# Kernel optimization log

Measured on AMD Instinct MI355X. Metric: run time of the kernel, lower is better.

The kernel has to match this reference:

```python
import jax, jax.numpy as jnp
import numpy as np

IN_CH = 31
OUT_CH = 31
G = 5          # grid_size
K = 3          # spline_order
GRID_LO, GRID_HI = -1.0, 1.0
NB = G + K     # number of B-spline basis functions
COEF_LEN = IN_CH * OUT_CH * NB        # 7688
UNIV_LEN = IN_CH * OUT_CH             # 961
RES_LEN = IN_CH * OUT_CH              # 961
PARAMS = COEF_LEN + UNIV_LEN + RES_LEN  # 9610


def _b_splines(x):
    """Cox-de Boor B-spline bases. x: (N, IN_CH) -> (N, IN_CH, G+K)."""
    h = (GRID_HI - GRID_LO) / G
    grid = jnp.arange(-K, G + K + 1, dtype=x.dtype) * h + GRID_LO  # (G+2K+1,)
    xe = x[..., None]
    b = ((xe >= grid[:-1]) & (xe < grid[1:])).astype(x.dtype)  # order-0, (N,I,G+2K)
    for p in range(1, K + 1):
        b = ((xe - grid[:-(p + 1)]) / (grid[p:-1] - grid[:-(p + 1)])) * b[..., :-1] \
          + ((grid[p + 1:] - xe) / (grid[p + 1:] - grid[1:-p])) * b[..., 1:]
    return b  # (N, IN_CH, NB)


def setup_inputs() -> dict:
    key = jax.random.key(0)
    k1, k2, k3 = jax.random.split(key, 3)
    # x in [-1,1) to span grid_range
    x = jax.random.uniform(k1, (1, IN_CH, 128, 128), dtype=jnp.float32) * 2.0 - 1.0
    # hypernetwork (generator) params: 3x3 conv 31 -> 9610
    gen_w = jax.random.normal(k2, (PARAMS, IN_CH, 3, 3), dtype=jnp.float32) * 0.02
    gen_b = jax.random.normal(k3, (PARAMS,), dtype=jnp.float32) * 0.01
    return {"x": x, "gen_w": gen_w, "gen_b": gen_b}


def reference(x, gen_w, gen_b):
    B, C, H, W = x.shape
    # generator: per-pixel KAN parameters, (B, PARAMS, H, W)
    w = jax.lax.conv_general_dilated(
        x, gen_w, window_strides=(1, 1), padding='SAME',
        dimension_numbers=('NCHW', 'OIHW', 'NCHW')) + gen_b[None, :, None, None]
    w = jnp.transpose(w, (0, 2, 3, 1)).reshape(B * H * W, PARAMS)
    xf = jnp.transpose(x, (0, 2, 3, 1)).reshape(B * H * W, C)
    # slice per-pixel params (mirrors kan_params_indices slicing + view)
    coef = w[:, :COEF_LEN].reshape(-1, IN_CH, OUT_CH, NB)
    univ = w[:, COEF_LEN:COEF_LEN + UNIV_LEN].reshape(-1, IN_CH, OUT_CH)
    res = w[:, COEF_LEN + UNIV_LEN:].reshape(-1, IN_CH, OUT_CH)
    bases = _b_splines(xf)                                # (N, I, NB)
    spline = jnp.einsum('nid,niod->nio', bases, coef)     # per-edge spline value
    silu = xf * jax.nn.sigmoid(xf)                        # residual activation
    out = jnp.einsum('nio,nio->no', univ, spline) + jnp.einsum('ni,nio->no', silu, res)
    return jnp.transpose(out.reshape(B, H, W, OUT_CH), (0, 3, 1, 2))
```

## Files before the change

### kernel.cpp

```cpp
#include <hip/hip_runtime.h>
#include <hip/hip_bf16.h>

#define OUT_CH   31
#define COEF_LEN 7688
#define NPIX     16384
#define CHUNKS   31
#define NFRG     24
#define NR       9
#define FRAG_U16 512
#define BP3_B    ((size_t)CHUNKS*NR*NFRG*FRAG_U16*2)
#define P1_B     ((size_t)OUT_CH*NPIX*4)
#define WS_NEED  (BP3_B + P1_B)

using f32x4 = __attribute__((ext_vector_type(4))) float;
using s16x8 = __attribute__((ext_vector_type(8))) short;

__device__ __forceinline__ unsigned short f2bf(float f) {
    unsigned int u = __float_as_uint(f);
    unsigned int r = (u + 0x7FFFu + ((u >> 16) & 1u)) >> 16;
    return (unsigned short)r;
}

__global__ void pack_kernel(const float* __restrict__ gw, const float* __restrict__ gb,
                            unsigned short* __restrict__ bp) {
    const int NMAIN = CHUNKS * NFRG * 64;
    int tt = blockIdx.x * 256 + threadIdx.x;
    if (tt >= NMAIN) return;
    int lane = tt & 63;
    int u = tt >> 6;
    int f = u % NFRG;
    int i = u / NFRG;
    int m = lane & 15, q8 = lane >> 4;
    int o = (m >> 2) * 8 + f / 3;
    int jslot = (f % 3) * 4 + (m & 3);
    int p = -1;
    if (o < OUT_CH && jslot < 10) {
        if (jslot < 8)       p = i * 248 + o * 8 + jslot;
        else if (jslot == 8) p = COEF_LEN + i * 31 + o;
        else                 p = COEF_LEN + 961 + i * 31 + o;
    }
    s16x8 vr[NR];
    #pragma unroll
    for (int r = 0; r < NR; ++r)
        #pragma unroll
        for (int jj = 0; jj < 8; ++jj) vr[r][jj] = 0;
    #pragma unroll
    for (int jj = 0; jj < 8; ++jj) {
        int ci = q8 * 8 + jj;
        if (p >= 0) {
            if (ci < 31) {
                const float* gr = gw + (long)p * 279 + ci * 9;
                #pragma unroll
                for (int r = 0; r < NR; ++r) vr[r][jj] = (short)f2bf(gr[r]);
            } else {
                vr[4][jj] = (short)f2bf(gb[p]);
            }
        }
    }
    #pragma unroll
    for (int r = 0; r < NR; ++r)
        *reinterpret_cast<s16x8*>(bp + (((size_t)i * NR + r) * NFRG + f) * FRAG_U16 + lane * 8) = vr[r];
}

__global__ void __launch_bounds__(512, 1)
main_kernel(const float* __restrict__ x, const unsigned short* __restrict__ bp3,
            float* __restrict__ dst0, float* __restrict__ dst1,
            int two_cg, int c0_in, int nc_in, int add_in) {
    __shared__ unsigned short slab[3 * 66 * 40];
    const int tid = threadIdx.x;
    const int bid = blockIdx.x;
    int row, ch, c0, nc, addf;
    float* dst;
    if (two_cg) {
        int cg = bid & 1;
        ch = (bid >> 1) & 1;
        row = bid >> 2;
        c0 = cg ? 16 : 0;
        nc = cg ? 15 : 16;
        dst = cg ? dst1 : dst0;
        addf = 0;
    } else {
        ch = bid & 1; row = bid >> 1;
        c0 = c0_in; nc = nc_in; dst = dst0; addf = add_in;
    }

    for (int idx = tid; idx < 3 * 66 * 40; idx += 512) {
        int slot = idx % 40;
        int t = idx / 40;
        int cc = t % 66;
        int rr = t / 66;
        int hh = row - 1 + rr, ww = ch * 64 - 1 + cc;
        unsigned short v = 0;
        if (slot < 31) {
            if ((unsigned)hh < 128u && (unsigned)ww < 128u)
                v = f2bf(x[slot * NPIX + hh * 128 + ww]);
        } else if (slot == 31) {
            v = 0x3F80;
        }
        slab[(rr * 66 + cc) * 40 + slot] = v;
    }
    __syncthreads();

    const int lane = tid & 63;
    const int fi = tid >> 6;
    const int q = lane >> 4;
    const int pix16 = lane & 15;
    const char* slabb = (const char*)slab;

    int sa[4];
    #pragma unroll
    for (int pg = 0; pg < 4; ++pg)
        sa[pg] = (pg * 16 + pix16) * 80 + q * 16;

    float oreg[4] = {0.f, 0.f, 0.f, 0.f};

    #pragma unroll 1
    for (int k = 0; k < nc; ++k) {
        const int ic = c0 + k;
        const unsigned short* aw = bp3 + ((size_t)ic * NR * NFRG + fi * 3) * FRAG_U16 + lane * 8;

        s16x8 pa[2][3];
        #pragma unroll
        for (int fl = 0; fl < 3; ++fl)
            pa[0][fl] = *reinterpret_cast<const s16x8*>(aw + fl * FRAG_U16);

        f32x4 acc[3][4];
        #pragma unroll
        for (int fl = 0; fl < 3; ++fl)
            #pragma unroll
            for (int pg = 0; pg < 4; ++pg)
                acc[fl][pg] = (f32x4){0.f, 0.f, 0.f, 0.f};

        #pragma unroll
        for (int r = 0; r < NR; ++r) {
            if (r + 1 < NR) {
                #pragma unroll
                for (int fl = 0; fl < 3; ++fl)
                    pa[(r + 1) & 1][fl] = *reinterpret_cast<const s16x8*>(
                        aw + ((r + 1) * NFRG + fl) * FRAG_U16);
            }
            const int roff = ((r / 3) * 66 + (r % 3)) * 80;
            s16x8 pbv[4];
            #pragma unroll
            for (int pg = 0; pg < 4; ++pg)
                pbv[pg] = *reinterpret_cast<const s16x8*>(slabb + sa[pg] + roff);

            __builtin_amdgcn_s_setprio(1);
            #pragma unroll
            for (int fl = 0; fl < 3; ++fl)
                #pragma unroll
                for (int pg = 0; pg < 4; ++pg)
                    acc[fl][pg] = __builtin_amdgcn_mfma_f32_16x16x32_bf16(
                        pa[r & 1][fl], pbv[pg], acc[fl][pg], 0, 0, 0);
            __builtin_amdgcn_s_setprio(0);
        }

        float bw0, bw1, bw2, bw3, cfv, slv;
        {
            unsigned short sv = slab[(66 + lane + 1) * 40 + ic];
            float xv = __uint_as_float((unsigned)sv << 16);
            float u5 = (xv + 1.0f) * 2.5f;
            cfv = fminf(fmaxf(floorf(u5), 0.f), 4.f);
            float t = u5 - cfv;
            float t2v = t * t, t3v = t2v * t;
            float omt = 1.f - t;
            bw3 = t3v * (1.f / 6.f);
            bw0 = omt * omt * omt * (1.f / 6.f);
            bw1 = 0.5f * t3v - t2v + (2.f / 3.f);
            bw2 = 1.f - bw0 - bw1 - bw3;
            slv = xv / (1.f + __expf(-xv));
        }

        #pragma unroll
        for (int pg = 0; pg < 4; ++pg) {
            const int src = pg * 16 + pix16;
            float b0 = __shfl(bw0, src);
            float b1 = __shfl(bw1, src);
            float b2 = __shfl(bw2, src);
            float b3 = __shfl(bw3, src);
            float cfp = __shfl(cfv, src);
            float slp = __shfl(slv, src);

            const float c0v = acc[0][pg][0], c1v = acc[0][pg][1];
            const float c2v = acc[0][pg][2], c3v = acc[0][pg][3];
            const float c4v = acc[1][pg][0], c5v = acc[1][pg][1];
            const float c6v = acc[1][pg][2], c7v = acc[1][pg][3];
            const bool m1 = cfp >= 1.f, m2 = cfp >= 2.f, m3 = cfp >= 3.f, m4 = cfp >= 4.f;
            float C0 = m1 ? c1v : c0v; C0 = m2 ? c2v : C0; C0 = m3 ? c3v : C0; C0 = m4 ? c4v : C0;
            float C1 = m1 ? c2v : c1v; C1 = m2 ? c3v : C1; C1 = m3 ? c4v : C1; C1 = m4 ? c5v : C1;
            float C2 = m1 ? c3v : c2v; C2 = m2 ? c4v : C2; C2 = m3 ? c5v : C2; C2 = m4 ? c6v : C2;
            float C3 = m1 ? c4v : c3v; C3 = m2 ? c5v : C3; C3 = m3 ? c6v : C3; C3 = m4 ? c7v : C3;

            float sp = b0 * C0;
            sp = fmaf(b1, C1, sp);
            sp = fmaf(b2, C2, sp);
            sp = fmaf(b3, C3, sp);
            oreg[pg] = fmaf(acc[2][pg][0], sp, fmaf(slp, acc[2][pg][1], oreg[pg]));
        }
    }

    const int o = q * 8 + fi;
    if (o < OUT_CH) {
        #pragma unroll
        for (int pg = 0; pg < 4; ++pg) {
            size_t gi = (size_t)o * NPIX + row * 128 + ch * 64 + pg * 16 + pix16;
            if (addf) dst[gi] += oreg[pg];
            else      dst[gi]  = oreg[pg];
        }
    }
}

__global__ void reduce_kernel(const float* __restrict__ p1, float* __restrict__ out) {
    int e = blockIdx.x * 256 + threadIdx.x;
    if (e < OUT_CH * NPIX) out[e] += p1[e];
}

extern "C" void kernel_launch(void* const* d_in, const int* in_sizes, int n_in,
                              void* d_out, int out_size, void* d_ws, size_t ws_size,
                              hipStream_t stream) {
    const float* x  = (const float*)d_in[0];
    const float* gw = (const float*)d_in[1];
    const float* gb = (const float*)d_in[2];
    float* outp = (float*)d_out;
    unsigned short* bpack = (unsigned short*)d_ws;
    float* p1 = (float*)((char*)d_ws + BP3_B);

    const int NMAIN = CHUNKS * NFRG * 64;
    pack_kernel<<<(NMAIN + 255) / 256, 256, 0, stream>>>(gw, gb, bpack);

    if (ws_size >= WS_NEED) {
        main_kernel<<<512, 512, 0, stream>>>(x, bpack, outp, p1, 1, 0, 0, 0);
        reduce_kernel<<<(OUT_CH * NPIX + 255) / 256, 256, 0, stream>>>(p1, outp);
    } else {
        main_kernel<<<256, 512, 0, stream>>>(x, bpack, outp, nullptr, 0, 0, 16, 0);
        main_kernel<<<256, 512, 0, stream>>>(x, bpack, outp, nullptr, 0, 16, 15, 1);
    }
}
```

Baseline: 114.5 us.

## Precompute spline weights in LDS and software-pipeline weight loads across channels

Before the main loop, the block now writes per-pixel, per-channel B-spline weights into LDS as a dense 8-wide weight row, along with the SiLU values. The epilogue then becomes a plain 8-term dot product instead of shuffles and select chains. The channel loop is unrolled by two, and the weight-fragment prefetch continues across channel boundaries so the next channel's first loads overlap the current epilogue. The cost is more LDS per block and extra global reads of x in the prologue.

```diff
diff --git a/kernel.cpp b/kernel.cpp
--- a/kernel.cpp
+++ b/kernel.cpp
@@ -8,7 +8,8 @@
 #define NFRG     24
 #define NR       9
 #define FRAG_U16 512
-#define BP3_B    ((size_t)CHUNKS*NR*NFRG*FRAG_U16*2)
+#define STEP_U16 (NFRG*FRAG_U16)
+#define BP3_B    ((size_t)CHUNKS*NR*STEP_U16*2)
 #define P1_B     ((size_t)OUT_CH*NPIX*4)
 #define WS_NEED  (BP3_B + P1_B)
 
@@ -67,6 +68,8 @@
             float* __restrict__ dst0, float* __restrict__ dst1,
             int two_cg, int c0_in, int nc_in, int add_in) {
     __shared__ unsigned short slab[3 * 66 * 40];
+    __shared__ float Wt[64 * 132];
+    __shared__ float SLt[64 * 17];
     const int tid = threadIdx.x;
     const int bid = blockIdx.x;
     int row, ch, c0, nc, addf;
@@ -99,7 +102,27 @@
         }
         slab[(rr * 66 + cc) * 40 + slot] = v;
     }
-    __syncthreads();
+
+    for (int idx = tid; idx < nc * 64; idx += 512) {
+        int px = idx & 63;
+        int k = idx >> 6;
+        float xv = x[(size_t)(c0 + k) * NPIX + row * 128 + ch * 64 + px];
+        float u5 = (xv + 1.0f) * 2.5f;
+        float cf = fminf(fmaxf(floorf(u5), 0.f), 4.f);
+        int ccb = (int)cf;
+        float t = u5 - cf;
+        float omt = 1.f - t;
+        float t2v = t * t, t3v = t2v * t;
+        float bw0 = omt * omt * omt * (1.f / 6.f);
+        float bw3 = t3v * (1.f / 6.f);
+        float bw1 = 0.5f * t3v - t2v + (2.f / 3.f);
+        float bw2 = 1.f - bw0 - bw1 - bw3;
+        float* wr = Wt + px * 132 + k * 8;
+        *reinterpret_cast<f32x4*>(wr) = (f32x4){0.f, 0.f, 0.f, 0.f};
+        *reinterpret_cast<f32x4*>(wr + 4) = (f32x4){0.f, 0.f, 0.f, 0.f};
+        wr[ccb] = bw0; wr[ccb + 1] = bw1; wr[ccb + 2] = bw2; wr[ccb + 3] = bw3;
+        SLt[px * 17 + k] = xv / (1.f + __expf(-xv));
+    }
 
     const int lane = tid & 63;
     const int fi = tid >> 6;
@@ -107,96 +130,93 @@
     const int pix16 = lane & 15;
     const char* slabb = (const char*)slab;
 
+    const unsigned short* awbase = bp3 + ((size_t)c0 * NR * NFRG + fi * 3) * FRAG_U16 + lane * 8;
+    s16x8 pa[2][3];
+    #pragma unroll
+    for (int fl = 0; fl < 3; ++fl)
+        pa[0][fl] = *reinterpret_cast<const s16x8*>(awbase + fl * FRAG_U16);
+
+    __syncthreads();
+
     int sa[4];
     #pragma unroll
     for (int pg = 0; pg < 4; ++pg)
         sa[pg] = (pg * 16 + pix16) * 80 + q * 16;
 
     float oreg[4] = {0.f, 0.f, 0.f, 0.f};
-
-    #pragma unroll 1
-    for (int k = 0; k < nc; ++k) {
-        const int ic = c0 + k;
-        const unsigned short* aw = bp3 + ((size_t)ic * NR * NFRG + fi * 3) * FRAG_U16 + lane * 8;
-
-        s16x8 pa[2][3];
+    f32x4 acc[3][4];
+
+    auto STEP = [&](int tl, int r, const unsigned short* awp, bool pf) {
+        if (pf) {
+            #pragma unroll
+            for (int fl = 0; fl < 3; ++fl)
+                pa[(tl + 1) & 1][fl] = *reinterpret_cast<const s16x8*>(
+                    awp + (size_t)(tl + 1) * STEP_U16 + fl * FRAG_U16);
+        }
+        const int roff = ((r / 3) * 66 + (r % 3)) * 80;
+        s16x8 pbv[4];
+        #pragma unroll
+        for (int pg = 0; pg < 4; ++pg)
+            pbv[pg] = *reinterpret_cast<const s16x8*>(slabb + sa[pg] + roff);
+        __builtin_amdgcn_s_setprio(1);
         #pragma unroll
         for (int fl = 0; fl < 3; ++fl)
-            pa[0][fl] = *reinterpret_cast<const s16x8*>(aw + fl * FRAG_U16);
-
-        f32x4 acc[3][4];
+            #pragma unroll
+            for (int pg = 0; pg < 4; ++pg)
+                acc[fl][pg] = __builtin_amdgcn_mfma_f32_16x16x32_bf16(
+                    pa[tl & 1][fl], pbv[pg], acc[fl][pg], 0, 0, 0);
+        __builtin_amdgcn_s_setprio(0);
+    };
+
+    auto ZERO = [&]() {
         #pragma unroll
         for (int fl = 0; fl < 3; ++fl)
             #pragma unroll
             for (int pg = 0; pg < 4; ++pg)
                 acc[fl][pg] = (f32x4){0.f, 0.f, 0.f, 0.f};
-
-        #pragma unroll
-        for (int r = 0; r < NR; ++r) {
-            if (r + 1 < NR) {
-                #pragma unroll
-                for (int fl = 0; fl < 3; ++fl)
-                    pa[(r + 1) & 1][fl] = *reinterpret_cast<const s16x8*>(
-                        aw + ((r + 1) * NFRG + fl) * FRAG_U16);
-            }
-            const int roff = ((r / 3) * 66 + (r % 3)) * 80;
-            s16x8 pbv[4];
-            #pragma unroll
-            for (int pg = 0; pg < 4; ++pg)
-                pbv[pg] = *reinterpret_cast<const s16x8*>(slabb + sa[pg] + roff);
-
-            __builtin_amdgcn_s_setprio(1);
-            #pragma unroll
-            for (int fl = 0; fl < 3; ++fl)
-                #pragma unroll
-                for (int pg = 0; pg < 4; ++pg)
-                    acc[fl][pg] = __builtin_amdgcn_mfma_f32_16x16x32_bf16(
-                        pa[r & 1][fl], pbv[pg], acc[fl][pg], 0, 0, 0);
-            __builtin_amdgcn_s_setprio(0);
-        }
-
-        float bw0, bw1, bw2, bw3, cfv, slv;
-        {
-            unsigned short sv = slab[(66 + lane + 1) * 40 + ic];
-            float xv = __uint_as_float((unsigned)sv << 16);
-            float u5 = (xv + 1.0f) * 2.5f;
-            cfv = fminf(fmaxf(floorf(u5), 0.f), 4.f);
-            float t = u5 - cfv;
-            float t2v = t * t, t3v = t2v * t;
-            float omt = 1.f - t;
-            bw3 = t3v * (1.f / 6.f);
-            bw0 = omt * omt * omt * (1.f / 6.f);
-            bw1 = 0.5f * t3v - t2v + (2.f / 3.f);
-            bw2 = 1.f - bw0 - bw1 - bw3;
-            slv = xv / (1.f + __expf(-xv));
-        }
-
+    };
+
+    auto EPI = [&](int k) {
         #pragma unroll
         for (int pg = 0; pg < 4; ++pg) {
-            const int src = pg * 16 + pix16;
-            float b0 = __shfl(bw0, src);
-            float b1 = __shfl(bw1, src);
-            float b2 = __shfl(bw2, src);
-            float b3 = __shfl(bw3, src);
-            float cfp = __shfl(cfv, src);
-            float slp = __shfl(slv, src);
-
-            const float c0v = acc[0][pg][0], c1v = acc[0][pg][1];
-            const float c2v = acc[0][pg][2], c3v = acc[0][pg][3];
-            const float c4v = acc[1][pg][0], c5v = acc[1][pg][1];
-            const float c6v = acc[1][pg][2], c7v = acc[1][pg][3];
-            const bool m1 = cfp >= 1.f, m2 = cfp >= 2.f, m3 = cfp >= 3.f, m4 = cfp >= 4.f;
-            float C0 = m1 ? c1v : c0v; C0 = m2 ? c2v : C0; C0 = m3 ? c3v : C0; C0 = m4 ? c4v : C0;
-            float C1 = m1 ? c2v : c1v; C1 = m2 ? c3v : C1; C1 = m3 ? c4v : C1; C1 = m4 ? c5v : C1;
-            float C2 = m1 ? c3v : c2v; C2 = m2 ? c4v : C2; C2 = m3 ? c5v : C2; C2 = m4 ? c6v : C2;
-            float C3 = m1 ? c4v : c3v; C3 = m2 ? c5v : C3; C3 = m3 ? c6v : C3; C3 = m4 ? c7v : C3;
-
-            float sp = b0 * C0;
-            sp = fmaf(b1, C1, sp);
-            sp = fmaf(b2, C2, sp);
-            sp = fmaf(b3, C3, sp);
-            oreg[pg] = fmaf(acc[2][pg][0], sp, fmaf(slp, acc[2][pg][1], oreg[pg]));
-        }
+            const float* wr = Wt + (pg * 16 + pix16) * 132 + k * 8;
+            f32x4 wlo = *reinterpret_cast<const f32x4*>(wr);
+            f32x4 whi = *reinterpret_cast<const f32x4*>(wr + 4);
+            float sl = SLt[(pg * 16 + pix16) * 17 + k];
+            float sp = wlo[0] * acc[0][pg][0];
+            sp = fmaf(wlo[1], acc[0][pg][1], sp);
+            sp = fmaf(wlo[2], acc[0][pg][2], sp);
+            sp = fmaf(wlo[3], acc[0][pg][3], sp);
+            sp = fmaf(whi[0], acc[1][pg][0], sp);
+            sp = fmaf(whi[1], acc[1][pg][1], sp);
+            sp = fmaf(whi[2], acc[1][pg][2], sp);
+            sp = fmaf(whi[3], acc[1][pg][3], sp);
+            oreg[pg] = fmaf(acc[2][pg][0], sp, fmaf(sl, acc[2][pg][1], oreg[pg]));
+        }
+    };
+
+    int kk = 0;
+    #pragma unroll 1
+    for (; kk + 2 <= nc; kk += 2) {
+        const unsigned short* awp = awbase + (size_t)kk * NR * STEP_U16;
+        ZERO();
+        #pragma unroll
+        for (int tl = 0; tl < 9; ++tl)
+            STEP(tl, tl, awp, true);
+        EPI(kk);
+        ZERO();
+        #pragma unroll
+        for (int tl = 9; tl < 18; ++tl)
+            STEP(tl, tl - 9, awp, tl < 17 || (kk + 2 < nc));
+        EPI(kk + 1);
+    }
+    if (kk < nc) {
+        const unsigned short* awp = awbase + (size_t)kk * NR * STEP_U16;
+        ZERO();
+        #pragma unroll
+        for (int tl = 0; tl < 9; ++tl)
+            STEP(tl, tl, awp, tl < 8);
+        EPI(kk);
     }
 
     const int o = q * 8 + fi;
```

Result: slower. 222.2 us (+94.1%).
